# Optimization experiments

Measured on AMD Instinct MI355X. Metric: run time of the kernel, lower is better.

## Reference

```python
import jax, jax.numpy as jnp
import numpy as np

B, NV, NF, E = 8, 2048, 4096, 12288
DIM, DCE, DCB, K = 512, 64, 192, 128
NQ, BITS, GROUPS = 2, 14, 8


def _conv1d(x, w, b):
    # x [B, C, N], w [O, I, 3]
    y = jax.lax.conv_general_dilated(x, w, (1,), [(1, 1)], dimension_numbers=('NCH', 'OIH', 'NCH'))
    return y + b[None, :, None]


def _group_norm(x, g, b, groups=GROUPS, eps=1e-5):
    B_, C, N = x.shape
    xg = x.reshape(B_, groups, C // groups, N)
    mu = xg.mean(axis=(2, 3), keepdims=True)
    var = xg.var(axis=(2, 3), keepdims=True)
    xn = ((xg - mu) * jax.lax.rsqrt(var + eps)).reshape(B_, C, N)
    return xn * g[None, :, None] + b[None, :, None]


def _block(x, w, bias, g, beta, m):
    x = x * m
    x = _conv1d(x, w, bias)
    x = x * m
    x = _group_norm(x, g, beta)
    return jax.nn.silu(x)


def _forward(vertices, coor_embed, W_in, b_in, sage_Wl, sage_Wr, sage_b, W_cb, b_cb,
             lfq_in, lfq_out, W_out, b_out, dec_conv_w, dec_conv_b, dec_gn_g, dec_gn_b,
             W_logits, b_logits, faces, face_edges, face_edges_mask, face_mask):
    lo, hi = -1.0, 1.0
    # discretize_coors
    disc = jnp.clip(jnp.round((vertices - lo) / (hi - lo) * K - 0.5), 0, K - 1).astype(jnp.int32)
    # gather per-face vertex coords: [b, nf, 3, 3] -> [b, nf, 9]
    fc = jax.vmap(lambda v, f: v[f])(disc, faces).reshape(B, NF, 9)
    emb = coor_embed[fc].reshape(B, NF, 9 * DCE)
    x = (emb @ W_in + b_in).reshape(B * NF, DIM)
    N = B * NF
    x = jnp.concatenate([x, jnp.zeros((1, DIM), x.dtype)], axis=0)  # pad node
    offset = (jnp.arange(B) * NF)[:, None, None]
    edges = jnp.where(face_edges_mask[:, None, :], face_edges + offset, N)
    edges = edges.transpose(1, 0, 2).reshape(2, -1)
    src, tgt = edges[0], edges[1]
    ones = jnp.ones(src.shape, x.dtype)
    for l in range(sage_Wl.shape[0]):  # SAGEConv, mean aggregation
        s = jax.ops.segment_sum(x[src], tgt, num_segments=N + 1)
        c = jax.ops.segment_sum(ones, tgt, num_segments=N + 1)
        x = (s / jnp.clip(c, 1.0)[:, None]) @ sage_Wl[l] + x @ sage_Wr[l] + sage_b[l]
    x = x[:-1].reshape(B, NF, DIM)
    # quantize path: scatter-mean face-corner embeddings onto vertices
    fe = (x @ W_cb + b_cb).reshape(B, NF * 3, DCB)
    faces_m = jnp.where(face_mask[:, :, None], faces, NV).reshape(B, NF * 3).astype(jnp.int32)
    num = jax.vmap(lambda e, i: jax.ops.segment_sum(e, i, num_segments=NV + 1))(fe, faces_m)
    den = jax.vmap(lambda i: jax.ops.segment_sum(jnp.ones((NF * 3,), fe.dtype), i, num_segments=NV + 1))(faces_m)
    avg = num / jnp.clip(den, 1e-5)[..., None]
    # residual lookup-free quantization with straight-through
    res, quant = avg, jnp.zeros_like(avg)
    for q in range(NQ):
        h = res @ lfq_in[q]
        bits = jnp.where(h > 0, 1.0, -1.0).astype(h.dtype)
        bits = h + jax.lax.stop_gradient(bits - h)
        outq = bits @ lfq_out[q]
        quant = quant + outq
        res = res - outq
    # gather quantized vertex codes back to faces
    feo = jax.vmap(lambda qv, i: qv[i])(quant, faces_m).reshape(B, NF, 3 * DCB)
    feo = feo @ W_out + b_out
    # conv resnet decoder
    xd = feo.transpose(0, 2, 1)  # [b, dim, nf]
    m = face_mask[:, None, :].astype(xd.dtype)
    for blk in range(dec_conv_w.shape[0]):
        h0 = xd
        for sub in range(2):
            h0 = _block(h0, dec_conv_w[blk, sub], dec_conv_b[blk, sub], dec_gn_g[blk, sub], dec_gn_b[blk, sub], m)
        xd = h0 + xd
    dec = xd.transpose(0, 2, 1)
    return (dec @ W_logits + b_logits).reshape(B, NF, 9, K)


def setup_inputs():
    key = jax.random.key(0)
    ks = jax.random.split(key, 24)
    r = lambda i, shape, s=0.02: jax.random.normal(ks[i], shape, jnp.float32) * s
    return dict(
        vertices=jax.random.uniform(ks[0], (B, NV, 3), jnp.float32, -0.95, 0.95),
        faces=jax.random.randint(ks[1], (B, NF, 3), 0, NV),
        face_edges=jax.random.randint(ks[2], (B, 2, E), 0, NF),
        face_edges_mask=jnp.ones((B, E), bool),
        face_mask=jnp.ones((B, NF), bool),
        coor_embed=r(3, (K, DCE), 1.0),
        W_in=r(4, (9 * DCE, DIM)), b_in=r(5, (DIM,)),
        sage_Wl=r(6, (2, DIM, DIM)), sage_Wr=r(7, (2, DIM, DIM)), sage_b=r(8, (2, DIM)),
        W_cb=r(9, (DIM, 3 * DCB)), b_cb=r(10, (3 * DCB,)),
        lfq_in=r(11, (NQ, DCB, BITS), 0.05), lfq_out=r(12, (NQ, BITS, DCB), 0.05),
        W_out=r(13, (3 * DCB, DIM)), b_out=r(14, (DIM,)),
        dec_conv_w=r(15, (2, 2, DIM, DIM, 3)), dec_conv_b=r(16, (2, 2, DIM)),
        dec_gn_g=jnp.ones((2, 2, DIM), jnp.float32), dec_gn_b=jnp.zeros((2, 2, DIM), jnp.float32),
        W_logits=r(17, (DIM, 9 * K)), b_logits=r(18, (9 * K,)),
    )


def reference(vertices, faces, face_edges, face_edges_mask, face_mask, coor_embed, W_in, b_in,
              sage_Wl, sage_Wr, sage_b, W_cb, b_cb, lfq_in, lfq_out, W_out, b_out,
              dec_conv_w, dec_conv_b, dec_gn_g, dec_gn_b, W_logits, b_logits):
    return _forward(vertices, coor_embed, W_in, b_in, sage_Wl, sage_Wr, sage_b, W_cb, b_cb,
                    lfq_in, lfq_out, W_out, b_out, dec_conv_w, dec_conv_b, dec_gn_g, dec_gn_b,
                    W_logits, b_logits, faces, face_edges, face_edges_mask, face_mask)
```

## Files before the change

### kernel.cpp

```cpp
#include <hip/hip_runtime.h>
#include <hip/hip_bf16.h>
#include <cstdint>
#include <cstddef>

constexpr int BB    = 8;
constexpr int NV    = 2048;
constexpr int NF    = 4096;
constexpr int NE    = 12288;
constexpr int DIM   = 512;
constexpr int DCB   = 192;
constexpr int NQv   = 2;
constexpr int BITSv = 14;
constexpr int NFACE = BB * NF;
constexpr int NEDGE = BB * NE;
constexpr int NVB   = BB * NV;
constexpr int NFP   = NF + 2;

typedef __attribute__((ext_vector_type(8))) short bf16x8;
typedef __attribute__((ext_vector_type(4))) float f32x4;

static __device__ __forceinline__ float b2f(unsigned short u) {
    union { unsigned u; float f; } x; x.u = ((unsigned)u) << 16; return x.f;
}
static __device__ __forceinline__ unsigned short f2bu(float v) {
    __hip_bfloat16 h = __float2bfloat16(v);
    return __builtin_bit_cast(unsigned short, h);
}
static __device__ __forceinline__ void split3(float v, unsigned short& a, unsigned short& b,
                                              unsigned short& c) {
    a = f2bu(v);            float r  = v - b2f(a);
    b = f2bu(r);            float r2 = r - b2f(b);
    c = f2bu(r2);
}
static __device__ __forceinline__ void load16(const void* g, void* l) {
    __builtin_amdgcn_global_load_lds((const __attribute__((address_space(1))) unsigned int*)g,
                                     (__attribute__((address_space(3))) unsigned int*)l, 16, 0, 0);
}

static __device__ __forceinline__ void xcd_swizzle(int& bx, int& by)
{
    const int nx  = (int)gridDim.x;
    const int lin = (int)(blockIdx.x + gridDim.x * blockIdx.y);
    const int xcd = lin & 7;
    const int j   = lin >> 3;
    bx = j % nx;
    by = xcd * 32 + j / nx;
}

__global__ void k_codes(const float* __restrict__ vertices, const int* __restrict__ faces,
                        int* __restrict__ fc)
{
    const int idx = blockIdx.x * 256 + threadIdx.x;
    if (idx >= NFACE * 9) return;
    const int r = idx / 9, p = idx - r * 9;
    const int i = p / 3, j = p - i * 3;
    const int b = r >> 12;
    const int v = faces[r * 3 + i];
    const float coord = vertices[((size_t)b * NV + v) * 3 + j];
    float t = rintf((coord + 1.0f) * 0.5f * 128.0f - 0.5f);
    t = fminf(fmaxf(t, 0.0f), 127.0f);
    fc[r * 12 + p] = (int)t;
}

__global__ __launch_bounds__(256)
void k_build_T(const float* __restrict__ ce, const float* __restrict__ W_in, float* __restrict__ T)
{
    const int p = blockIdx.x;
    const int c = blockIdx.y;
    const int o = threadIdx.x * 2;
    float s0 = 0.f, s1 = 0.f;
    for (int d = 0; d < 64; ++d) {
        const float e = ce[c * 64 + d];
        const float* wr_ = W_in + (size_t)(p * 64 + d) * 512 + o;
        s0 = fmaf(e, wr_[0], s0);
        s1 = fmaf(e, wr_[1], s1);
    }
    float* dst = T + ((size_t)p * 128 + c) * 512 + o;
    dst[0] = s0; dst[1] = s1;
}

__global__ __launch_bounds__(256)
void k_xin(const int* __restrict__ fc, const float* __restrict__ T,
           const float* __restrict__ b_in,
           unsigned short* __restrict__ x0, unsigned short* __restrict__ x1,
           unsigned short* __restrict__ x2)
{
    const int r = blockIdx.x;
    const int o = threadIdx.x * 2;
    float s0 = b_in[o], s1 = b_in[o + 1];
#pragma unroll
    for (int p = 0; p < 9; ++p) {
        const int c = fc[r * 12 + p];
        const float* t = T + ((size_t)p * 128 + c) * 512 + o;
        s0 += t[0]; s1 += t[1];
    }
    unsigned short h0, m0, l0, h1, m1, l1;
    split3(s0, h0, m0, l0); split3(s1, h1, m1, l1);
    const size_t ob = (size_t)r * 512 + o;
    ushort2 u;
    u.x = h0; u.y = h1; *(ushort2*)&x0[ob] = u;
    u.x = m0; u.y = m1; *(ushort2*)&x1[ob] = u;
    u.x = l0; u.y = l1; *(ushort2*)&x2[ob] = u;
}

__global__ void k_count_e(const int* __restrict__ fe, int* __restrict__ deg)
{
    const int e = blockIdx.x * 256 + threadIdx.x;
    if (e >= NEDGE) return;
    const int b = e / NE, ee = e - b * NE;
    atomicAdd(&deg[fe[(b * 2 + 1) * NE + ee] + b * NF], 1);
}
__global__ void k_fill_e(const int* __restrict__ fe, int* __restrict__ cursor, int* __restrict__ srcE)
{
    const int e = blockIdx.x * 256 + threadIdx.x;
    if (e >= NEDGE) return;
    const int b = e / NE, ee = e - b * NE;
    const int src = fe[(b * 2 + 0) * NE + ee] + b * NF;
    const int tgt = fe[(b * 2 + 1) * NE + ee] + b * NF;
    srcE[atomicAdd(&cursor[tgt], 1)] = src;
}
__global__ void k_count_v(const int* __restrict__ faces, int* __restrict__ deg)
{
    const int q = blockIdx.x * 256 + threadIdx.x;
    if (q >= NEDGE) return;
    atomicAdd(&deg[(q / (NF * 3)) * NV + faces[q]], 1);
}
__global__ void k_fill_v(const int* __restrict__ faces, int* __restrict__ cursor, int* __restrict__ cid)
{
    const int q = blockIdx.x * 256 + threadIdx.x;
    if (q >= NEDGE) return;
    const int b = q / (NF * 3);
    cid[atomicAdd(&cursor[b * NV + faces[q]], 1)] = q;
}
__global__ void k_scan(const int* __restrict__ deg, int* __restrict__ rowstart,
                       int* __restrict__ cursor, int n)
{
    __shared__ int part[256];
    const int t = threadIdx.x;
    const int chunk = n / 256;
    int s = 0;
    for (int i = 0; i < chunk; ++i) s += deg[t * chunk + i];
    part[t] = s;
    __syncthreads();
    for (int o = 1; o < 256; o <<= 1) {
        int v = (t >= o) ? part[t - o] : 0;
        __syncthreads();
        part[t] += v;
        __syncthreads();
    }
    int base = (t == 0) ? 0 : part[t - 1];
    for (int i = 0; i < chunk; ++i) {
        const int idx = t * chunk + i;
        const int d = deg[idx];
        rowstart[idx] = base;
        cursor[idx]   = base;
        base += d;
    }
    if (t == 255) rowstart[n] = base;
}

__global__ void k_agg_e3(const unsigned short* __restrict__ p0, const unsigned short* __restrict__ p1,
                         const unsigned short* __restrict__ p2, const int* __restrict__ rowstart,
                         const int* __restrict__ srcE,
                         unsigned short* __restrict__ o0, unsigned short* __restrict__ o1,
                         unsigned short* __restrict__ o2)
{
    const int t = threadIdx.x;
    const int r = blockIdx.x * 2 + (t >> 7);
    const int c4 = (t & 127) << 2;
    const int s = rowstart[r], e = rowstart[r + 1];
    float a0 = 0.f, a1 = 0.f, a2 = 0.f, a3 = 0.f;
    for (int i = s; i < e; ++i) {
        const size_t ba = (size_t)srcE[i] * 512 + c4;
        const ushort4 u0 = *(const ushort4*)(p0 + ba);
        const ushort4 u1 = *(const ushort4*)(p1 + ba);
        const ushort4 u2 = *(const ushort4*)(p2 + ba);
        a0 += b2f(u0.x) + b2f(u1.x) + b2f(u2.x);
        a1 += b2f(u0.y) + b2f(u1.y) + b2f(u2.y);
        a2 += b2f(u0.z) + b2f(u1.z) + b2f(u2.z);
        a3 += b2f(u0.w) + b2f(u1.w) + b2f(u2.w);
    }
    const float inv = 1.0f / fmaxf((float)(e - s), 1.0f);
    a0 *= inv; a1 *= inv; a2 *= inv; a3 *= inv;
    ushort4 q0, q1, q2;
    split3(a0, q0.x, q1.x, q2.x); split3(a1, q0.y, q1.y, q2.y);
    split3(a2, q0.z, q1.z, q2.z); split3(a3, q0.w, q1.w, q2.w);
    const size_t ob = (size_t)r * 512 + c4;
    *(ushort4*)(o0 + ob) = q0; *(ushort4*)(o1 + ob) = q1; *(ushort4*)(o2 + ob) = q2;
}

__global__ void k_agg_verts(const float* __restrict__ fe, const int* __restrict__ rowstart,
                            const int* __restrict__ cid, float* __restrict__ avg)
{
    const int r = blockIdx.x;
    const int c = threadIdx.x;
    const int s = rowstart[r], e = rowstart[r + 1];
    float a = 0.f;
    for (int i = s; i < e; ++i) {
        const int q = cid[i];
        const int face = q / 3, corner = q - face * 3;
        a += fe[(size_t)face * 576 + corner * 192 + c];
    }
    avg[(size_t)r * 192 + c] = a / fmaxf((float)(e - s), 1e-5f);
}

__global__ void k_lfq(const float* __restrict__ avg, const float* __restrict__ lfq_in,
                      const float* __restrict__ lfq_out, float* __restrict__ quant)
{
    __shared__ float res[DCB];
    __shared__ float qacc[DCB];
    __shared__ float bits[BITSv];
    const int r = blockIdx.x;
    const int t = threadIdx.x;
    for (int c = t; c < DCB; c += 64) {
        res[c]  = avg[(size_t)r * DCB + c];
        qacc[c] = 0.f;
    }
    __syncthreads();
    for (int q = 0; q < NQv; ++q) {
        if (t < BITSv) {
            float h = 0.f;
            const float* w = lfq_in + q * DCB * BITSv + t;
            for (int k = 0; k < DCB; ++k) h += res[k] * w[k * BITSv];
            bits[t] = (h > 0.f) ? 1.f : -1.f;
        }
        __syncthreads();
        for (int c = t; c < DCB; c += 64) {
            float o = 0.f;
            const float* w2 = lfq_out + q * BITSv * DCB + c;
#pragma unroll
            for (int j = 0; j < BITSv; ++j) o += bits[j] * w2[j * DCB];
            qacc[c] += o;
            res[c]  -= o;
        }
        __syncthreads();
    }
    for (int c = t; c < DCB; c += 64) quant[(size_t)r * DCB + c] = qacc[c];
}

__global__ void k_gather_feo(const float* __restrict__ quant, const int* __restrict__ faces,
                             unsigned short* __restrict__ feo)
{
    const long long idx = (long long)blockIdx.x * 256 + threadIdx.x;
    if (idx >= (long long)NFACE * 576) return;
    const int row = (int)(idx / 576);
    const int col = (int)(idx - (long long)row * 576);
    const int i = col / 192, c = col - i * 192;
    const int b = row >> 12;
    const int v = faces[row * 3 + i];
    feo[idx] = f2bu(quant[((size_t)b * NV + v) * 192 + c]);
}

__global__ void k_pack_plain(const float* __restrict__ src, unsigned short* __restrict__ dst,
                             int Kd, int Nd)
{
    const int idx = blockIdx.x * 256 + threadIdx.x;
    if (idx >= Kd * Nd) return;
    const int n = idx / Kd, k = idx - n * Kd;
    dst[idx] = f2bu(src[(size_t)k * Nd + n]);
}
__global__ void k_pack_conv(const float* __restrict__ w, unsigned short* __restrict__ bt)
{
    const int idx = blockIdx.x * 256 + threadIdx.x;
    if (idx >= 4 * 512 * 1536) return;
    const int ws_ = idx / (512 * 1536);
    const int rem = idx - ws_ * 512 * 1536;
    const int o = rem / 1536, k = rem - o * 1536;
    const int tap = k >> 9, i = k & 511;
    bt[idx] = f2bu(w[(((size_t)(ws_ * 512 + o)) * 512 + i) * 3 + tap]);
}
static __device__ __forceinline__ unsigned short bplane(float w, int inner)
{
    unsigned short w0, w1, w2; split3(w, w0, w1, w2);
    const int bsel = (inner == 3) ? 2 : ((inner == 1 || inner == 4) ? 1 : 0);
    return (bsel == 0) ? w0 : ((bsel == 1) ? w1 : w2);
}
__global__ void k_pack_sage3(const float* __restrict__ wl, const float* __restrict__ wr,
                             unsigned short* __restrict__ bt)
{
    const int idx = blockIdx.x * 256 + threadIdx.x;
    if (idx >= 2 * 512 * 6144) return;
    const int l = idx / (512 * 6144);
    const int rem = idx - l * 512 * 6144;
    const int n = rem / 6144, k = rem - n * 6144;
    const int seg = k >> 9, kk = k & 511;
    const int inner = (seg >= 6) ? seg - 6 : seg;
    const float* W = ((seg >= 6) ? wr : wl) + (size_t)l * 512 * 512;
    bt[idx] = bplane(W[kk * 512 + n], inner);
}
__global__ void k_pack_cb3(const float* __restrict__ w, unsigned short* __restrict__ bt)
{
    const int idx = blockIdx.x * 256 + threadIdx.x;
    if (idx >= 640 * 3072) return;
    const int n = idx / 3072, k = idx - n * 3072;
    const int seg = k >> 9, kk = k & 511;
    const float v = (n < 576) ? w[kk * 576 + n] : 0.f;
    bt[idx] = bplane(v, seg);
}

__global__ void k_zero_guards(unsigned short* __restrict__ xdp, unsigned short* __restrict__ hp)
{
    const int idx = blockIdx.x * 256 + threadIdx.x;
    if (idx >= 8192) return;
    const int b = idx >> 10, rem = idx & 1023;
    const int row = (rem >> 9) ? (NF + 1) : 0;
    const int c = rem & 511;
    const size_t o = ((size_t)b * NFP + row) * 512 + c;
    xdp[o] = 0; hp[o] = 0;
}

template <int NSEG, int OUTE>
__global__ __launch_bounds__(256)
void k_mm_enc(const unsigned short* __restrict__ g0, const unsigned short* __restrict__ g1,
              const unsigned short* __restrict__ g2, const unsigned short* __restrict__ xA0,
              const unsigned short* __restrict__ xA1, const unsigned short* __restrict__ xA2,
              const unsigned short* __restrict__ Bt, const float* __restrict__ bias,
              void* __restrict__ C0, void* __restrict__ C1, void* __restrict__ C2, int N)
{
    constexpr int K = NSEG * 512;
    constexpr int NGRP = (NSEG == 12) ? 6 : 3;
    __shared__ __align__(16) short As[128 * 32];
    __shared__ __align__(16) short Bs[3][128 * 32];

    int bx, by;
    xcd_swizzle(bx, by);
    const int t  = threadIdx.x;
    const int m0 = by * 128;
    const int n0 = bx * 128;
    const int w  = t >> 6, l = t & 63;
    const int wr = w >> 1, wc = w & 1;
    const int lr = l & 15, lq = l >> 4;

    f32x4 acc[4][4];
#pragma unroll
    for (int i = 0; i < 4; ++i)
#pragma unroll
        for (int j = 0; j < 4; ++j)
#pragma unroll
            for (int r = 0; r < 4; ++r) acc[i][j][r] = 0.f;

    const unsigned short* const APL[6] = {g0, g1, g2, xA0, xA1, xA2};
    constexpr int SB[7]  = {0, 3, 5, 6, 9, 11, 12};
    constexpr int SL[12] = {0, 1, 3, 2, 4, 5, 6, 7, 9, 8, 10, 11};

#pragma unroll 1
    for (int kk = 0; kk < 512; kk += 32) {
#pragma unroll
        for (int grp = 0; grp < NGRP; ++grp) {
            const unsigned short* Ab = APL[grp];
            const int ns = SB[grp + 1] - SB[grp];
#pragma unroll
            for (int half = 0; half < 2; ++half) {
                const int ch = (half << 8) + t;
                const int row = ch >> 2, kq = ch & 3;
                load16(Ab + (size_t)(m0 + row) * 512 + kk + kq * 8, &As[ch * 8]);
#pragma unroll
                for (int s = 0; s < 3; ++s) {
                    if (s < ns) {
                        const int seg = SL[SB[grp] + s];
                        load16(Bt + (size_t)(n0 + row) * K + seg * 512 + kk + kq * 8,
                               &Bs[s][ch * 8]);
                    }
                }
            }
            __syncthreads();
            bf16x8 aF[4];
#pragma unroll
            for (int i = 0; i < 4; ++i)
                aF[i] = *(const bf16x8*)&As[(wr * 64 + i * 16 + lr) * 32 + lq * 8];
#pragma unroll
            for (int s = 0; s < 3; ++s) {
                if (s < ns) {
                    bf16x8 bF[4];
#pragma unroll
                    for (int j = 0; j < 4; ++j)
                        bF[j] = *(const bf16x8*)&Bs[s][(wc * 64 + j * 16 + lr) * 32 + lq * 8];
#pragma unroll
                    for (int i = 0; i < 4; ++i)
#pragma unroll
                        for (int j = 0; j < 4; ++j)
                            acc[i][j] = __builtin_amdgcn_mfma_f32_16x16x32_bf16(aF[i], bF[j],
                                                                                acc[i][j], 0, 0, 0);
                }
            }
            __syncthreads();
        }
    }

#pragma unroll
    for (int i = 0; i < 4; ++i) {
#pragma unroll
        for (int r = 0; r < 4; ++r) {
            const int m = m0 + wr * 64 + i * 16 + lq * 4 + r;
#pragma unroll
            for (int j = 0; j < 4; ++j) {
                const int n = n0 + wc * 64 + j * 16 + lr;
                if (OUTE == 0) {
                    const float v = acc[i][j][r] + bias[n];
                    unsigned short u0, u1, u2; split3(v, u0, u1, u2);
                    const size_t ob = (size_t)m * 512 + n;
                    ((unsigned short*)C0)[ob] = u0;
                    ((unsigned short*)C1)[ob] = u1;
                    ((unsigned short*)C2)[ob] = u2;
                } else {
                    if (n < N) ((float*)C0)[(size_t)m * N + n] = acc[i][j][r] + bias[n];
                }
            }
        }
    }
}

template <int AMODE, int OUT>
__global__ __launch_bounds__(256)
void k_mm(const unsigned short* __restrict__ a0, const unsigned short* __restrict__ Bt,
          const float* __restrict__ bias, void* __restrict__ C0, int N, int K)
{
    __shared__ __align__(16) short As[128 * 32];
    __shared__ __align__(16) short Bs[128 * 32];

    int bx, by;
    xcd_swizzle(bx, by);
    const int t  = threadIdx.x;
    const int m0 = by * 128;
    const int n0 = bx * 128;
    const int w  = t >> 6, l = t & 63;
    const int wr = w >> 1, wc = w & 1;
    const int lr = l & 15, lq = l >> 4;

    f32x4 acc[4][4];
#pragma unroll
    for (int i = 0; i < 4; ++i)
#pragma unroll
        for (int j = 0; j < 4; ++j)
#pragma unroll
            for (int r = 0; r < 4; ++r) acc[i][j][r] = 0.f;

    for (int k0 = 0; k0 < K; k0 += 32) {
#pragma unroll
        for (int half = 0; half < 2; ++half) {
            const int ch = (half << 8) + t;
            const int row = ch >> 2, kq = ch & 3;
            const int m = m0 + row;
            const unsigned short* ga;
            if (AMODE == 0) {
                ga = a0 + (size_t)m * K + k0 + kq * 8;
            } else if (AMODE == 1) {
                ga = a0 + (((size_t)(m + ((m >> 12) << 1) + 1)) << 9) + k0 + kq * 8;
            } else {
                const int tap = k0 >> 9;
                ga = a0 + (((size_t)(m + ((m >> 12) << 1) + tap)) << 9) + (k0 & 511) + kq * 8;
            }
            load16(ga, &As[ch * 8]);
            load16(Bt + (size_t)(n0 + row) * K + k0 + kq * 8, &Bs[ch * 8]);
        }
        __syncthreads();

        bf16x8 aF[4], bF[4];
#pragma unroll
        for (int i = 0; i < 4; ++i) {
            aF[i] = *(const bf16x8*)&As[(wr * 64 + i * 16 + lr) * 32 + lq * 8];
            bF[i] = *(const bf16x8*)&Bs[(wc * 64 + i * 16 + lr) * 32 + lq * 8];
        }
#pragma unroll
        for (int i = 0; i < 4; ++i)
#pragma unroll
            for (int j = 0; j < 4; ++j)
                acc[i][j] = __builtin_amdgcn_mfma_f32_16x16x32_bf16(aF[i], bF[j], acc[i][j], 0, 0, 0);
        __syncthreads();
    }

#pragma unroll
    for (int i = 0; i < 4; ++i) {
#pragma unroll
        for (int r = 0; r < 4; ++r) {
            const int m = m0 + wr * 64 + i * 16 + lq * 4 + r;
#pragma unroll
            for (int j = 0; j < 4; ++j) {
                const int n = n0 + wc * 64 + j * 16 + lr;
                const float bv = (OUT == 1) ? ((n < N) ? bias[n] : 0.f) : bias[n];
                const float v = acc[i][j][r] + bv;
                if (OUT == 0) {
                    ((unsigned short*)C0)[(size_t)m * 512 + n] = f2bu(v);
                } else if (OUT == 1) {
                    if (n < N) ((float*)C0)[(size_t)m * N + n] = v;
                } else {
                    ((unsigned short*)C0)[((size_t)(m + ((m >> 12) << 1) + 1)) * 512 + n] = f2bu(v);
                }
            }
        }
    }
}

__global__ __launch_bounds__(256)
void k_gn_stats(const unsigned short* __restrict__ h, float* __restrict__ stats)
{
    const int bg = blockIdx.x;
    const int b = bg >> 3, g = bg & 7;
    const int t = threadIdx.x;
    float sum = 0.f, sq = 0.f;
    const unsigned short* base = h + (size_t)b * NF * 512 + g * 64;
    for (int n = t; n < NF; n += 256) {
        const unsigned short* p = base + (size_t)n * 512;
#pragma unroll
        for (int c = 0; c < 64; c += 4) {
            const ushort4 v4 = *(const ushort4*)(p + c);
            const float f0 = b2f(v4.x), f1 = b2f(v4.y), f2 = b2f(v4.z), f3 = b2f(v4.w);
            sum += f0 + f1 + f2 + f3;
            sq  += f0 * f0 + f1 * f1 + f2 * f2 + f3 * f3;
        }
    }
    __shared__ float s1[256], s2[256];
    s1[t] = sum; s2[t] = sq;
    __syncthreads();
    for (int o = 128; o > 0; o >>= 1) {
        if (t < o) { s1[t] += s1[t + o]; s2[t] += s2[t + o]; }
        __syncthreads();
    }
    if (t == 0) {
        const float cntf = (float)(NF * 64);
        const float mean = s1[0] / cntf;
        const float var  = s2[0] / cntf - mean * mean;
        stats[bg * 2 + 0] = mean;
        stats[bg * 2 + 1] = rsqrtf(var + 1e-5f);
    }
}

__global__ void k_gn_apply(const unsigned short* __restrict__ h, const float* __restrict__ stats,
                           const float* __restrict__ gamma, const float* __restrict__ beta,
                           const unsigned short* __restrict__ resid_pad, unsigned short* __restrict__ dst_pad)
{
    const int idx = blockIdx.x * 256 + threadIdx.x;
    if (idx >= NFACE * 512 / 4) return;
    const int i4 = idx * 4;
    const int c = i4 & 511;
    const int row = i4 >> 9;
    const int b = row >> 12;
    const int g = c >> 6;
    const float mean = stats[(b * 8 + g) * 2 + 0];
    const float rstd = stats[(b * 8 + g) * 2 + 1];
    const ushort4 v4 = *(const ushort4*)(h + (size_t)row * 512 + c);
    const float4 gm = *(const float4*)&gamma[c];
    const float4 bt = *(const float4*)&beta[c];
    float o0 = (b2f(v4.x) - mean) * rstd * gm.x + bt.x;
    float o1 = (b2f(v4.y) - mean) * rstd * gm.y + bt.y;
    float o2 = (b2f(v4.z) - mean) * rstd * gm.z + bt.z;
    float o3 = (b2f(v4.w) - mean) * rstd * gm.w + bt.w;
    o0 = o0 / (1.f + expf(-o0));
    o1 = o1 / (1.f + expf(-o1));
    o2 = o2 / (1.f + expf(-o2));
    o3 = o3 / (1.f + expf(-o3));
    const size_t po = ((size_t)row + (size_t)(row >> 12) * 2 + 1) * 512 + c;
    if (resid_pad) {
        const ushort4 r4 = *(const ushort4*)(resid_pad + po);
        o0 += b2f(r4.x); o1 += b2f(r4.y); o2 += b2f(r4.z); o3 += b2f(r4.w);
    }
    ushort4 o;
    o.x = f2bu(o0); o.y = f2bu(o1); o.z = f2bu(o2); o.w = f2bu(o3);
    *(ushort4*)(dst_pad + po) = o;
}

extern "C" void kernel_launch(void* const* d_in, const int* in_sizes, int n_in,
                              void* d_out, int out_size, void* d_ws, size_t ws_size,
                              hipStream_t stream)
{
    const float* vertices   = (const float*)d_in[0];
    const int*   faces      = (const int*)  d_in[1];
    const int*   face_edges = (const int*)  d_in[2];
    const float* coor_embed = (const float*)d_in[5];
    const float* W_in    = (const float*)d_in[6];
    const float* b_in    = (const float*)d_in[7];
    const float* sage_Wl = (const float*)d_in[8];
    const float* sage_Wr = (const float*)d_in[9];
    const float* sage_b  = (const float*)d_in[10];
    const float* W_cb    = (const float*)d_in[11];
    const float* b_cb    = (const float*)d_in[12];
    const float* lfq_in  = (const float*)d_in[13];
    const float* lfq_out = (const float*)d_in[14];
    const float* W_out   = (const float*)d_in[15];
    const float* b_out   = (const float*)d_in[16];
    const float* dconv_w = (const float*)d_in[17];
    const float* dconv_b = (const float*)d_in[18];
    const float* dgn_g   = (const float*)d_in[19];
    const float* dgn_b   = (const float*)d_in[20];
    const float* W_log   = (const float*)d_in[21];
    const float* b_log   = (const float*)d_in[22];

    char* base = (char*)d_ws;
    size_t off = 0;
    auto alloc = [&](size_t bytes) { char* p = base + off; off += (bytes + 255) & ~(size_t)255; return p; };

    const size_t PLANE  = (size_t)NFACE * 512 * 2;
    char* P1 = alloc(3 * PLANE);
    char* P2 = alloc(3 * PLANE);
    char* P3 = alloc(3 * PLANE + 65536);

    unsigned short* x0 = (unsigned short*)P1;
    unsigned short* x1 = x0 + (size_t)NFACE * 512;
    unsigned short* x2 = x1 + (size_t)NFACE * 512;
    unsigned short* g0 = (unsigned short*)P2;
    unsigned short* g1 = g0 + (size_t)NFACE * 512;
    unsigned short* g2 = g1 + (size_t)NFACE * 512;
    unsigned short* y0 = (unsigned short*)P3;
    unsigned short* y1 = y0 + (size_t)NFACE * 512;
    unsigned short* y2 = y1 + (size_t)NFACE * 512;
    float*          fe   = (float*)P3;
    unsigned short* feo  = (unsigned short*)P2;
    float*          avg  = (float*)(P2 + (size_t)40 * 1024 * 1024);
    float*          quant = avg + (size_t)NVB * 192;
    unsigned short* xdp  = (unsigned short*)P3;
    unsigned short* hp   = xdp + (size_t)BB * NFP * 512;
    unsigned short* cbuf = hp + (size_t)BB * NFP * 512;

    int*   fc = (int*)  alloc((size_t)NFACE * 12 * 4);
    float* T  = (float*)alloc((size_t)9 * 128 * 512 * 4);
    unsigned short* bt_sage = (unsigned short*)alloc(2ull * 512 * 6144 * 2);
    unsigned short* bt_cb   = (unsigned short*)alloc(640ull * 3072 * 2);
    unsigned short* bt_out  = (unsigned short*)alloc(512ull * 576 * 2);
    unsigned short* bt_log  = (unsigned short*)alloc(1152ull * 512 * 2);
    unsigned short* bt_conv = (unsigned short*)alloc(4ull * 512 * 1536 * 2);
    int* degE = (int*)alloc(32768 * 4);
    int* rsE  = (int*)alloc(32772 * 4);
    int* curE = (int*)alloc(32768 * 4);
    int* srcE = (int*)alloc(98304 * 4);
    int* degV = (int*)alloc(16384 * 4);
    int* rsV  = (int*)alloc(16388 * 4);
    int* curV = (int*)alloc(16384 * 4);
    int* cidV = (int*)alloc(98304 * 4);
    float* stats = (float*)alloc(128 * 4);

    const dim3 blk(256);

    k_pack_sage3<<<dim3(24576), blk, 0, stream>>>(sage_Wl, sage_Wr, bt_sage);
    k_pack_cb3  <<<dim3(7680),  blk, 0, stream>>>(W_cb, bt_cb);
    k_pack_plain<<<dim3(1152),  blk, 0, stream>>>(W_out, bt_out, 576, 512);
    k_pack_plain<<<dim3(2304),  blk, 0, stream>>>(W_log, bt_log, 512, 1152);
    k_pack_conv <<<dim3(12288), blk, 0, stream>>>(dconv_w, bt_conv);

    hipMemsetAsync(degE, 0, 32768 * 4, stream);
    hipMemsetAsync(degV, 0, 16384 * 4, stream);
    k_count_e<<<dim3(384), blk, 0, stream>>>(face_edges, degE);
    k_count_v<<<dim3(384), blk, 0, stream>>>(faces, degV);
    k_scan<<<dim3(1), blk, 0, stream>>>(degE, rsE, curE, 32768);
    k_scan<<<dim3(1), blk, 0, stream>>>(degV, rsV, curV, 16384);
    k_fill_e<<<dim3(384), blk, 0, stream>>>(face_edges, curE, srcE);
    k_fill_v<<<dim3(384), blk, 0, stream>>>(faces, curV, cidV);

    k_codes<<<dim3(1152), blk, 0, stream>>>(vertices, faces, fc);
    k_build_T<<<dim3(9, 128), blk, 0, stream>>>(coor_embed, W_in, T);
    k_xin<<<dim3(NFACE), blk, 0, stream>>>(fc, T, b_in, x0, x1, x2);

    k_agg_e3<<<dim3(16384), blk, 0, stream>>>(x0, x1, x2, rsE, srcE, g0, g1, g2);
    k_mm_enc<12, 0><<<dim3(4, 256), blk, 0, stream>>>(g0, g1, g2, x0, x1, x2,
        bt_sage, sage_b, y0, y1, y2, 512);

    k_agg_e3<<<dim3(16384), blk, 0, stream>>>(y0, y1, y2, rsE, srcE, g0, g1, g2);
    k_mm_enc<12, 0><<<dim3(4, 256), blk, 0, stream>>>(g0, g1, g2, y0, y1, y2,
        bt_sage + (size_t)512 * 6144, sage_b + 512, x0, x1, x2, 512);

    k_mm_enc<6, 1><<<dim3(5, 256), blk, 0, stream>>>(x0, x1, x2, nullptr, nullptr, nullptr,
        bt_cb, b_cb, fe, nullptr, nullptr, 576);

    k_agg_verts<<<dim3(NVB), dim3(192), 0, stream>>>(fe, rsV, cidV, avg);
    k_lfq<<<dim3(NVB), dim3(64), 0, stream>>>(avg, lfq_in, lfq_out, quant);
    k_gather_feo<<<dim3(73728), blk, 0, stream>>>(quant, faces, feo);

    k_zero_guards<<<dim3(32), blk, 0, stream>>>(xdp, hp);
    k_mm<0, 2><<<dim3(4, 256), blk, 0, stream>>>(feo, bt_out, b_out, xdp, 512, 576);

    for (int blkI = 0; blkI < 2; ++blkI) {
        k_mm<2, 0><<<dim3(4, 256), blk, 0, stream>>>(xdp,
            bt_conv + (size_t)(blkI * 2 + 0) * 512 * 1536, dconv_b + (blkI * 2 + 0) * 512,
            cbuf, 512, 1536);
        k_gn_stats<<<dim3(64), blk, 0, stream>>>(cbuf, stats);
        k_gn_apply<<<dim3(16384), blk, 0, stream>>>(cbuf, stats,
            dgn_g + (blkI * 2 + 0) * 512, dgn_b + (blkI * 2 + 0) * 512, nullptr, hp);
        k_mm<2, 0><<<dim3(4, 256), blk, 0, stream>>>(hp,
            bt_conv + (size_t)(blkI * 2 + 1) * 512 * 1536, dconv_b + (blkI * 2 + 1) * 512,
            cbuf, 512, 1536);
        k_gn_stats<<<dim3(64), blk, 0, stream>>>(cbuf, stats);
        k_gn_apply<<<dim3(16384), blk, 0, stream>>>(cbuf, stats,
            dgn_g + (blkI * 2 + 1) * 512, dgn_b + (blkI * 2 + 1) * 512, xdp, xdp);
    }

    k_mm<1, 1><<<dim3(9, 256), blk, 0, stream>>>(xdp, bt_log, b_log, (float*)d_out, 1152, 512);
}
```

Before: 1.937 ms.

## Add dedicated conv1d GEMM reusing shifted A tile across three taps

Replaces the generic GEMM for the decoder conv1d layers with a specialised kernel. Each K-step loads a single 130-row A tile from the padded activation buffer plus three B tiles, one per tap, and reads the A tile at row offsets 0, 1 and 2 from shared memory. The generic path appears to treat the conv as a K=1536 GEMM that reloads shifted A rows for every tap, so the new kernel cuts global and LDS traffic for A. In exchange it uses more shared memory per block, which may reduce occupancy, and keeps no double buffering.

Result: faster. 1.838 ms (-5.1%).

```diff
diff --git a/kernel.cpp b/kernel.cpp
--- a/kernel.cpp
+++ b/kernel.cpp
@@ -486,6 +486,85 @@
                 } else {
                     ((unsigned short*)C0)[((size_t)(m + ((m >> 12) << 1) + 1)) * 512 + n] = f2bu(v);
                 }
+            }
+        }
+    }
+}
+
+__global__ __launch_bounds__(256)
+void k_mm_conv(const unsigned short* __restrict__ ap, const unsigned short* __restrict__ Bt,
+               const float* __restrict__ bias, unsigned short* __restrict__ C0)
+{
+    __shared__ __align__(16) short As[132 * 32];
+    __shared__ __align__(16) short Bs[3][128 * 32];
+
+    int bx, by;
+    xcd_swizzle(bx, by);
+    const int t  = threadIdx.x;
+    const int m0 = by * 128;
+    const int n0 = bx * 128;
+    const int w  = t >> 6, l = t & 63;
+    const int wr = w >> 1, wc = w & 1;
+    const int lr = l & 15, lq = l >> 4;
+    const int pbase = m0 + ((m0 >> 12) << 1);
+
+    f32x4 acc[4][4];
+#pragma unroll
+    for (int i = 0; i < 4; ++i)
+#pragma unroll
+        for (int j = 0; j < 4; ++j)
+#pragma unroll
+            for (int r = 0; r < 4; ++r) acc[i][j][r] = 0.f;
+
+#pragma unroll 1
+    for (int kk = 0; kk < 512; kk += 32) {
+#pragma unroll
+        for (int rnd = 0; rnd < 2; ++rnd) {
+            const int ch = (rnd << 8) + t;
+            const int row = ch >> 2, kq = ch & 3;
+            load16(ap + (((size_t)(pbase + row)) << 9) + kk + kq * 8, &As[ch * 8]);
+        }
+        if (t < 8) {
+            const int ch = 512 + t;
+            const int row = ch >> 2, kq = ch & 3;
+            load16(ap + (((size_t)(pbase + row)) << 9) + kk + kq * 8, &As[ch * 8]);
+        }
+#pragma unroll
+        for (int tap = 0; tap < 3; ++tap) {
+#pragma unroll
+            for (int half = 0; half < 2; ++half) {
+                const int ch = (half << 8) + t;
+                const int row = ch >> 2, kq = ch & 3;
+                load16(Bt + (size_t)(n0 + row) * 1536 + tap * 512 + kk + kq * 8, &Bs[tap][ch * 8]);
+            }
+        }
+        __syncthreads();
+#pragma unroll
+        for (int tap = 0; tap < 3; ++tap) {
+            bf16x8 aF[4], bF[4];
+#pragma unroll
+            for (int i = 0; i < 4; ++i) {
+                aF[i] = *(const bf16x8*)&As[(tap + wr * 64 + i * 16 + lr) * 32 + lq * 8];
+                bF[i] = *(const bf16x8*)&Bs[tap][(wc * 64 + i * 16 + lr) * 32 + lq * 8];
+            }
+#pragma unroll
+            for (int i = 0; i < 4; ++i)
+#pragma unroll
+                for (int j = 0; j < 4; ++j)
+                    acc[i][j] = __builtin_amdgcn_mfma_f32_16x16x32_bf16(aF[i], bF[j], acc[i][j], 0, 0, 0);
+        }
+        __syncthreads();
+    }
+
+#pragma unroll
+    for (int i = 0; i < 4; ++i) {
+#pragma unroll
+        for (int r = 0; r < 4; ++r) {
+            const int m = m0 + wr * 64 + i * 16 + lq * 4 + r;
+#pragma unroll
+            for (int j = 0; j < 4; ++j) {
+                const int n = n0 + wc * 64 + j * 16 + lr;
+                C0[(size_t)m * 512 + n] = f2bu(acc[i][j][r] + bias[n]);
             }
         }
     }
@@ -668,15 +747,13 @@
     k_mm<0, 2><<<dim3(4, 256), blk, 0, stream>>>(feo, bt_out, b_out, xdp, 512, 576);
 
     for (int blkI = 0; blkI < 2; ++blkI) {
-        k_mm<2, 0><<<dim3(4, 256), blk, 0, stream>>>(xdp,
-            bt_conv + (size_t)(blkI * 2 + 0) * 512 * 1536, dconv_b + (blkI * 2 + 0) * 512,
-            cbuf, 512, 1536);
+        k_mm_conv<<<dim3(4, 256), blk, 0, stream>>>(xdp,
+            bt_conv + (size_t)(blkI * 2 + 0) * 512 * 1536, dconv_b + (blkI * 2 + 0) * 512, cbuf);
         k_gn_stats<<<dim3(64), blk, 0, stream>>>(cbuf, stats);
         k_gn_apply<<<dim3(16384), blk, 0, stream>>>(cbuf, stats,
             dgn_g + (blkI * 2 + 0) * 512, dgn_b + (blkI * 2 + 0) * 512, nullptr, hp);
-        k_mm<2, 0><<<dim3(4, 256), blk, 0, stream>>>(hp,
-            bt_conv + (size_t)(blkI * 2 + 1) * 512 * 1536, dconv_b + (blkI * 2 + 1) * 512,
-            cbuf, 512, 1536);
+        k_mm_conv<<<dim3(4, 256), blk, 0, stream>>>(hp,
+            bt_conv + (size_t)(blkI * 2 + 1) * 512 * 1536, dconv_b + (blkI * 2 + 1) * 512, cbuf);
         k_gn_stats<<<dim3(64), blk, 0, stream>>>(cbuf, stats);
         k_gn_apply<<<dim3(16384), blk, 0, stream>>>(cbuf, stats,
             dgn_g + (blkI * 2 + 1) * 512, dgn_b + (blkI * 2 + 1) * 512, xdp, xdp);
```
